# Kernel tuning notes

Measured on AMD Instinct MI355X. Metric: run time of the kernel, lower is better.

Reference implementation:

```python
import jax, jax.numpy as jnp
import numpy as np
from jax import lax

B, T = 8192, 2048
INIT_ALPHA = 0.1


def setup_inputs() -> dict:
    key = jax.random.key(0)
    kx, = jax.random.split(key, 1)
    # intermittent demand: small non-negative integers, many exact zeros
    x = jax.random.randint(kx, (B, T), 0, 3).astype(jnp.float32)
    alpha = jnp.full((1, 1), INIT_ALPHA, dtype=jnp.float32)  # learned smoothing weight
    Z0 = jnp.ones((B,), dtype=jnp.float32)  # demand-size state
    V0 = jnp.ones((B,), dtype=jnp.float32)  # inter-demand-interval state
    q0 = jnp.ones((B,), dtype=jnp.float32)  # periods since last nonzero demand
    return {"x": x, "alpha": alpha, "Z0": Z0, "V0": V0, "q0": q0}


def reference(x, alpha, Z0, V0, q0):
    """Croston's method recurrence (sba=False): out_t = Z_t / V_t.

    x: (B, T) demand series; states are per-series scalars carried through a scan.
    """
    a = alpha[0, 0]

    def step(carry, xt):  # xt: (B,)
        Z, V, q = carry
        Z_next = a * xt + (1.0 - a) * Z
        V_next = a * q + (1.0 - a) * V
        nz = xt != 0.0
        Z_next = jnp.where(nz, Z_next, Z)
        V_next = jnp.where(nz, V_next, V)
        q_next = jnp.where(nz, 1.0, q + 1.0)
        out = Z_next / V_next  # sba=False branch
        return (Z_next, V_next, q_next), out

    _, outs = lax.scan(step, (Z0, V0, q0), x.T)  # outs: (T, B)
    return outs.T  # (B, T)
```

## Files before the change

kernel.cpp:

```cpp
#include <hip/hip_runtime.h>
#include <stdint.h>


#define TLEN 2048
#define CH   64
#define WARM 128
#define NCH  (TLEN / CH)
#define TW   32
#define LROW 33

typedef float vf4 __attribute__((ext_vector_type(4)));

#define GLDS16(gp, lp)                                                        \
    __builtin_amdgcn_global_load_lds(                                         \
        (const __attribute__((address_space(1))) uint32_t*)(gp),              \
        (__attribute__((address_space(3))) uint32_t*)(lp), 16, 0, 0)

__global__ __launch_bounds__(128) void croston_kernel(
    const float* __restrict__ x,
    const float* __restrict__ alpha,
    const float* __restrict__ Z0,
    const float* __restrict__ V0,
    const float* __restrict__ q0,
    float* __restrict__ out)
{
    __shared__ float ring[2][2][64 * TW];
    __shared__ float outb[2][64 * LROW];

    const int warp = threadIdx.x >> 6;
    const int lane = threadIdx.x & 63;

    const int xr = blockIdx.x & 7;
    const int bm = blockIdx.x >> 3;
    const int sg = xr * 16 + (bm & 15);
    const int c  = (bm >> 4) * 2 + warp;

    const int sbase = sg * 64;
    const int s     = c * CH;

    const float a  = alpha[0];
    const float ma = 1.0f - a;

    const int t_start = (s >= WARM) ? (s - WARM) : 0;
    const int ntiles  = (s + CH - t_start) / TW;

    float Z, V, q;
    if (t_start == 0) {
        Z = Z0[sbase + lane];
        V = V0[sbase + lane];
        q = q0[sbase + lane];
    } else {
        Z = 1.0f; V = 1.0f; q = 1.0f;
    }

    const int rho  = lane >> 3;
    const int kap  = lane & 7;
    const int mrot = ((kap + rho) & 7) * 4;

    float* ring0 = ring[warp][0];
    float* ring1 = ring[warp][1];
    float* ob    = outb[warp];

    auto dma_tile = [&](float* slot, int t0) {
        const float* gbase = x + (size_t)(sbase + rho) * TLEN + t0 + mrot;
        #pragma unroll
        for (int i = 0; i < 8; ++i)
            GLDS16(gbase + (size_t)i * 8 * TLEN, slot + i * 256);
    };

    auto step = [&](float xt) {
        const bool  nz = (xt != 0.0f);
        const float Zn = fmaf(ma, Z, a * xt);
        const float Vn = fmaf(ma, V, a * q);
        Z = nz ? Zn : Z;
        V = nz ? Vn : V;
        q = nz ? 1.0f : q + 1.0f;
    };

    dma_tile(ring0, t_start);
    dma_tile(ring1, t_start + TW);

    const int srot = lane & 7;

    for (int t = 0; t < ntiles; ++t) {
        float* slot = (t & 1) ? ring1 : ring0;
        const int t0 = t_start + t * TW;

        asm volatile("s_waitcnt vmcnt(8)" ::: "memory");

        vf4 v[8];
        #pragma unroll
        for (int mm = 0; mm < 8; ++mm)
            v[mm] = *(const vf4*)(slot + lane * 32 + (((mm - srot) & 7) << 2));

        asm volatile("s_waitcnt lgkmcnt(0)" ::: "memory");
        if (t + 2 < ntiles) dma_tile(slot, t0 + 2 * TW);

        if (t0 >= s) {
            #pragma unroll
            for (int mm = 0; mm < 8; ++mm) {
                #pragma unroll
                for (int k = 0; k < 4; ++k) {
                    step(v[mm][k]);
                    v[mm][k] = Z * __builtin_amdgcn_rcpf(V);
                }
            }
            #pragma unroll
            for (int mm = 0; mm < 8; ++mm) {
                #pragma unroll
                for (int k = 0; k < 4; ++k)
                    ob[lane * LROW + 4 * mm + k] = v[mm][k];
            }
            asm volatile("s_waitcnt lgkmcnt(0)" ::: "memory");
            #pragma unroll
            for (int i = 0; i < 8; ++i) {
                const float* p = ob + (i * 8 + rho) * LROW + (kap << 2);
                vf4 o4;
                o4.x = p[0]; o4.y = p[1]; o4.z = p[2]; o4.w = p[3];
                __builtin_nontemporal_store(
                    o4, (vf4*)(out + (size_t)(sbase + i * 8 + rho) * TLEN + t0 + (kap << 2)));
            }
        } else {
            #pragma unroll
            for (int mm = 0; mm < 8; ++mm) {
                #pragma unroll
                for (int k = 0; k < 4; ++k) step(v[mm][k]);
            }
        }
    }
}

extern "C" void kernel_launch(void* const* d_in, const int* in_sizes, int n_in,
                              void* d_out, int out_size, void* d_ws, size_t ws_size,
                              hipStream_t stream) {
    const float* x     = (const float*)d_in[0];
    const float* alpha = (const float*)d_in[1];
    const float* Z0    = (const float*)d_in[2];
    const float* V0    = (const float*)d_in[3];
    const float* q0    = (const float*)d_in[4];
    float* out = (float*)d_out;

    dim3 block(128);
    dim3 grid(2048);
    croston_kernel<<<grid, block, 0, stream>>>(x, alpha, Z0, V0, q0, out);
}
```

Baseline: 130.0 us.

## Double chunk length to cut warm-up rereads and reuse input ring for transpose

Each wave now emits 128 timesteps instead of 64, with the same 128-step warm-up. That cuts redundant input reads and warm-up recurrence work per output, and halves the grid. The separate output staging buffer is removed: results are written back into the input ring slot for the transpose before the global stores. The tile loop is fully unrolled with per-tile wait counts, and refill is deferred until after the tile's compute and stores. Costs: longer serial chains per wave, fewer waves to hide latency, and less prefetch overlap because refills are issued later.

```diff
diff --git a/kernel.cpp b/kernel.cpp
--- a/kernel.cpp
+++ b/kernel.cpp
@@ -3,11 +3,10 @@
 
 
 #define TLEN 2048
-#define CH   64
+#define CH   128
 #define WARM 128
 #define NCH  (TLEN / CH)
 #define TW   32
-#define LROW 33
 
 typedef float vf4 __attribute__((ext_vector_type(4)));
 
@@ -15,6 +14,46 @@
     __builtin_amdgcn_global_load_lds(                                         \
         (const __attribute__((address_space(1))) uint32_t*)(gp),              \
         (__attribute__((address_space(3))) uint32_t*)(lp), 16, 0, 0)
+
+#define TILE(T, NWAIT, EMIT, REFILL) do {                                     \
+    float* slot = ((T) & 1) ? ring1 : ring0;                                  \
+    const int t0 = t_start + (T) * TW;                                        \
+    asm volatile("s_waitcnt vmcnt(" #NWAIT ")" ::: "memory");                 \
+    vf4 v[8];                                                                 \
+    _Pragma("unroll")                                                         \
+    for (int mm = 0; mm < 8; ++mm)                                            \
+        v[mm] = *(const vf4*)(slot + lane * 32 + (((mm - k8) & 7) << 2));     \
+    asm volatile("s_waitcnt lgkmcnt(0)" ::: "memory");                        \
+    if (EMIT) {                                                               \
+        _Pragma("unroll")                                                     \
+        for (int mm = 0; mm < 8; ++mm) {                                      \
+            _Pragma("unroll")                                                 \
+            for (int k = 0; k < 4; ++k) {                                     \
+                step(v[mm][k]);                                               \
+                v[mm][k] = Z * __builtin_amdgcn_rcpf(V);                      \
+            }                                                                 \
+        }                                                                     \
+        _Pragma("unroll")                                                     \
+        for (int mm = 0; mm < 8; ++mm)           \
+            *(vf4*)(slot + lane * 32 + (((mm - k8) & 7) << 2)) = v[mm];       \
+        asm volatile("s_waitcnt lgkmcnt(0)" ::: "memory");                    \
+        _Pragma("unroll")                                                     \
+        for (int i = 0; i < 8; ++i) {                \
+            const float* p = slot + (i * 8 + rho) * 32 + (((k8 - rho) & 7) << 2); \
+            vf4 o4; o4.x = p[0]; o4.y = p[1]; o4.z = p[2]; o4.w = p[3];       \
+            __builtin_nontemporal_store(                                      \
+                o4, (vf4*)(out + (size_t)(sbase + i * 8 + rho) * TLEN + t0 + (k8 << 2))); \
+        }                                                                     \
+        asm volatile("s_waitcnt lgkmcnt(0)" ::: "memory");                    \
+    } else {                                                                  \
+        _Pragma("unroll")                                                     \
+        for (int mm = 0; mm < 8; ++mm) {                                      \
+            _Pragma("unroll")                                                 \
+            for (int k = 0; k < 4; ++k) step(v[mm][k]);                       \
+        }                                                                     \
+    }                                                                         \
+    if (REFILL) dma_tile(slot, t0 + 2 * TW);     \
+} while (0)
 
 __global__ __launch_bounds__(128) void croston_kernel(
     const float* __restrict__ x,
@@ -25,7 +64,6 @@
     float* __restrict__ out)
 {
     __shared__ float ring[2][2][64 * TW];
-    __shared__ float outb[2][64 * LROW];
 
     const int warp = threadIdx.x >> 6;
     const int lane = threadIdx.x & 63;
@@ -37,15 +75,13 @@
 
     const int sbase = sg * 64;
     const int s     = c * CH;
+    const int t_start = (c == 0) ? 0 : (s - WARM);
 
     const float a  = alpha[0];
     const float ma = 1.0f - a;
 
-    const int t_start = (s >= WARM) ? (s - WARM) : 0;
-    const int ntiles  = (s + CH - t_start) / TW;
-
     float Z, V, q;
-    if (t_start == 0) {
+    if (c == 0) {
         Z = Z0[sbase + lane];
         V = V0[sbase + lane];
         q = q0[sbase + lane];
@@ -53,13 +89,12 @@
         Z = 1.0f; V = 1.0f; q = 1.0f;
     }
 
-    const int rho  = lane >> 3;
-    const int kap  = lane & 7;
-    const int mrot = ((kap + rho) & 7) * 4;
+    const int rho = lane >> 3;
+    const int k8  = lane & 7;
+    const int mrot = ((k8 + rho) & 7) * 4;
 
     float* ring0 = ring[warp][0];
     float* ring1 = ring[warp][1];
-    float* ob    = outb[warp];
 
     auto dma_tile = [&](float* slot, int t0) {
         const float* gbase = x + (size_t)(sbase + rho) * TLEN + t0 + mrot;
@@ -80,53 +115,20 @@
     dma_tile(ring0, t_start);
     dma_tile(ring1, t_start + TW);
 
-    const int srot = lane & 7;
-
-    for (int t = 0; t < ntiles; ++t) {
-        float* slot = (t & 1) ? ring1 : ring0;
-        const int t0 = t_start + t * TW;
-
-        asm volatile("s_waitcnt vmcnt(8)" ::: "memory");
-
-        vf4 v[8];
-        #pragma unroll
-        for (int mm = 0; mm < 8; ++mm)
-            v[mm] = *(const vf4*)(slot + lane * 32 + (((mm - srot) & 7) << 2));
-
-        asm volatile("s_waitcnt lgkmcnt(0)" ::: "memory");
-        if (t + 2 < ntiles) dma_tile(slot, t0 + 2 * TW);
-
-        if (t0 >= s) {
-            #pragma unroll
-            for (int mm = 0; mm < 8; ++mm) {
-                #pragma unroll
-                for (int k = 0; k < 4; ++k) {
-                    step(v[mm][k]);
-                    v[mm][k] = Z * __builtin_amdgcn_rcpf(V);
-                }
-            }
-            #pragma unroll
-            for (int mm = 0; mm < 8; ++mm) {
-                #pragma unroll
-                for (int k = 0; k < 4; ++k)
-                    ob[lane * LROW + 4 * mm + k] = v[mm][k];
-            }
-            asm volatile("s_waitcnt lgkmcnt(0)" ::: "memory");
-            #pragma unroll
-            for (int i = 0; i < 8; ++i) {
-                const float* p = ob + (i * 8 + rho) * LROW + (kap << 2);
-                vf4 o4;
-                o4.x = p[0]; o4.y = p[1]; o4.z = p[2]; o4.w = p[3];
-                __builtin_nontemporal_store(
-                    o4, (vf4*)(out + (size_t)(sbase + i * 8 + rho) * TLEN + t0 + (kap << 2)));
-            }
-        } else {
-            #pragma unroll
-            for (int mm = 0; mm < 8; ++mm) {
-                #pragma unroll
-                for (int k = 0; k < 4; ++k) step(v[mm][k]);
-            }
-        }
+    if (c == 0) {
+        TILE(0,  8, 1, 1);
+        TILE(1, 16, 1, 1);
+        TILE(2, 16, 1, 0);
+        TILE(3,  8, 1, 0);
+    } else {
+        TILE(0,  8, 0, 1);
+        TILE(1,  8, 0, 1);
+        TILE(2,  8, 0, 1);
+        TILE(3,  8, 0, 1);
+        TILE(4,  8, 1, 1);
+        TILE(5, 16, 1, 1);
+        TILE(6, 16, 1, 0);
+        TILE(7,  8, 1, 0);
     }
 }
 
@@ -141,6 +143,6 @@
     float* out = (float*)d_out;
 
     dim3 block(128);
-    dim3 grid(2048);
+    dim3 grid(1024);
     croston_kernel<<<grid, block, 0, stream>>>(x, alpha, Z0, V0, q0, out);
 }
```

Result: faster. 127.4 us (-2.0%).
